# Kernel tuning notes

Hardware: AMD Instinct MI355X
Metric: run time of the kernel (lower is better)

## Reference

```python
import jax, jax.numpy as jnp
import numpy as np


def setup_inputs() -> dict:
    key = jax.random.key(0)
    k1, k2 = jax.random.split(key)
    B, N, M, D = 8, 8192, 8192, 3
    x = jax.random.normal(k1, (B, N, D), dtype=jnp.float32)
    y = jax.random.normal(k2, (B, M, D), dtype=jnp.float32)
    return {"x": x, "y": y}


def reference(x, y):
    # dist[b, i, j] = |x_bi|^2 + |y_bj|^2 - 2 * <x_bi, y_bj>
    # (same math as the torch code's rx.transpose(2,1) + ry - 2*xy, but
    #  computed with row-norm vectors instead of full NxN / MxM bmms)
    xx = jnp.sum(x * x, axis=-1)                      # [B, N]
    yy = jnp.sum(y * y, axis=-1)                      # [B, M]
    xy = jnp.einsum('bnd,bmd->bnm', x, y)             # [B, N, M]
    dist = xx[:, :, None] + yy[:, None, :] - 2.0 * xy # [B, N, M]
    dist1 = jnp.min(dist, axis=1)  # min over x points -> per-y nearest  [B, M]
    dist2 = jnp.min(dist, axis=2)  # min over y points -> per-x nearest  [B, N]
    return jnp.mean(dist1) + jnp.mean(dist2)
```

## Files before the change

kernel.cpp:

```cpp
#include <hip/hip_runtime.h>


#define B_ 8
#define N_ 8192
#define PTS (B_ * N_)
#define TPB 512

typedef short bf16x8 __attribute__((ext_vector_type(8)));
typedef float f32x16 __attribute__((ext_vector_type(16)));

__device__ __forceinline__ unsigned b16(float f) {
  unsigned u = __float_as_uint(f);
  return (u + 0x7FFFu + ((u >> 16) & 1u)) >> 16;
}
__device__ __forceinline__ float bf(unsigned h) { return __uint_as_float(h << 16); }

__device__ __forceinline__ void build_chunk(const float* __restrict__ cb,
                                            uint4* __restrict__ dst, int t) {
  const unsigned one = 0x3F80u;
#pragma unroll
  for (int q = 0; q < 2; ++q) {
    int p = t + q * TPB;
    float c0 = cb[3 * p], c1 = cb[3 * p + 1], c2 = cb[3 * p + 2];
    float nc = fmaf(c0, c0, fmaf(c1, c1, c2 * c2));
    unsigned yh0 = b16(c0), yh1 = b16(c1), yh2 = b16(c2);
    unsigned yl0 = b16(c0 - bf(yh0)), yl1 = b16(c1 - bf(yh1)), yl2 = b16(c2 - bf(yh2));
    unsigned nh = b16(nc), nl = b16(nc - bf(nh));
    int tt = p >> 5, mm = p & 31;
    dst[tt * 64 + mm]      = make_uint4(yh0 | (yh1 << 16), yh2 | (yl0 << 16),
                                        yl1 | (yl2 << 16), yh0 | (yh1 << 16));
    dst[tt * 64 + 32 + mm] = make_uint4(yh2 | (one << 16), one | (nh << 16),
                                        nl, 0u);
  }
}

__global__ __launch_bounds__(TPB, 4) void chamfer_main_k(
    const float* __restrict__ x, const float* __restrict__ y,
    float* __restrict__ gpart) {
  __shared__ uint4 ldsFrag[2][32 * 64];

  const unsigned one = 0x3F80u;
  int t = threadIdx.x, lane = t & 63, w = t >> 6;
  int b = blockIdx.x;
  int g = b >> 1;
  int hf = b & 1;
  int dir = g >> 7;
  int gg = g & 127;
  int batch = gg >> 4;
  int seg = gg & 15;
  const float* __restrict__ own  = dir ? y : x;
  const float* __restrict__ cand = dir ? x : y;

  int m = lane & 31;
  int rowBase = batch * N_ + seg * 512 + w * 64;
  bf16x8 A0, A1;
#pragma unroll
  for (int a = 0; a < 2; ++a) {
    const float* po = own + 3 * (rowBase + a * 32 + m);
    float v0 = po[0], v1 = po[1], v2 = po[2];
    float nv = fmaf(v0, v0, fmaf(v1, v1, v2 * v2));
    float a0 = -2.0f * v0, a1 = -2.0f * v1, a2 = -2.0f * v2;
    unsigned ah0 = b16(a0), ah1 = b16(a1), ah2 = b16(a2);
    unsigned al0 = b16(a0 - bf(ah0)), al1 = b16(a1 - bf(ah1)), al2 = b16(a2 - bf(ah2));
    unsigned nh = b16(nv), nl = b16(nv - bf(nh));
    uint4 h0 = make_uint4(ah0 | (ah1 << 16), ah2 | (ah0 << 16),
                          ah1 | (ah2 << 16), al0 | (al1 << 16));
    uint4 h1 = make_uint4(al2 | (nh << 16), nl | (one << 16), one, 0u);
    uint4 afr;
    afr.x = (lane < 32) ? h0.x : h1.x;
    afr.y = (lane < 32) ? h0.y : h1.y;
    afr.z = (lane < 32) ? h0.z : h1.z;
    afr.w = (lane < 32) ? h0.w : h1.w;
    if (a == 0) A0 = __builtin_bit_cast(bf16x8, afr);
    else        A1 = __builtin_bit_cast(bf16x8, afr);
  }

  f32x16 z = {0.f,0.f,0.f,0.f,0.f,0.f,0.f,0.f,0.f,0.f,0.f,0.f,0.f,0.f,0.f,0.f};
  f32x16 rm0, rm1;
#pragma unroll
  for (int r = 0; r < 16; ++r) { rm0[r] = 1e30f; rm1[r] = 1e30f; }

  const float* cbb = cand + (batch * N_ + hf * 4096) * 3;
  build_chunk(cbb, ldsFrag[0], t);
  __syncthreads();

  for (int ch = 0; ch < 4; ++ch) {
    const uint4* cur = ldsFrag[ch & 1];
    if (ch < 3)
      build_chunk(cbb + (ch + 1) * 1024 * 3, ldsFrag[(ch + 1) & 1], t);

#pragma unroll 2
    for (int i = 0; i < 16; ++i) {
      bf16x8 B0 = __builtin_bit_cast(bf16x8, cur[(2 * i) * 64 + lane]);
      bf16x8 B1 = __builtin_bit_cast(bf16x8, cur[(2 * i + 1) * 64 + lane]);
      f32x16 acc0 = __builtin_amdgcn_mfma_f32_32x32x16_bf16(A0, B0, z, 0, 0, 0);
      f32x16 acc1 = __builtin_amdgcn_mfma_f32_32x32x16_bf16(A1, B0, z, 0, 0, 0);
      f32x16 acc2 = __builtin_amdgcn_mfma_f32_32x32x16_bf16(A0, B1, z, 0, 0, 0);
      f32x16 acc3 = __builtin_amdgcn_mfma_f32_32x32x16_bf16(A1, B1, z, 0, 0, 0);
#pragma unroll
      for (int r = 0; r < 16; ++r) {
        rm0[r] = fminf(fminf(rm0[r], acc0[r]), acc2[r]);
        rm1[r] = fminf(fminf(rm1[r], acc1[r]), acc3[r]);
      }
    }
    __syncthreads();
  }

#pragma unroll
  for (int msk = 1; msk <= 16; msk <<= 1)
#pragma unroll
    for (int r = 0; r < 16; ++r) {
      rm0[r] = fminf(rm0[r], __shfl_xor(rm0[r], msk, 64));
      rm1[r] = fminf(rm1[r], __shfl_xor(rm1[r], msk, 64));
    }

  float* gp = gpart + b * 512;
  if ((lane & 31) == 0) {
    int h = lane >> 5;
#pragma unroll
    for (int r = 0; r < 16; ++r) {
      int rr = (r & 3) + 8 * (r >> 2) + 4 * h;
      gp[w * 64 + rr] = rm0[r];
      gp[w * 64 + 32 + rr] = rm1[r];
    }
  }
}

__global__ __launch_bounds__(256) void chamfer_final_k(
    const float* __restrict__ gpart, float* __restrict__ out) {
  int i = blockIdx.x * 256 + threadIdx.x;
  float s = 0.0f;
#pragma unroll
  for (int e = 0; e < 4; ++e) {
    int rowid = 4 * i + e;
    int g = rowid >> 9, r = rowid & 511;
    s += fminf(gpart[(2 * g) * 512 + r], gpart[(2 * g + 1) * 512 + r]);
  }
  for (int off = 32; off > 0; off >>= 1) s += __shfl_down(s, off, 64);
  __shared__ float red[4];
  int lane = threadIdx.x & 63, wv = threadIdx.x >> 6;
  if (lane == 0) red[wv] = s;
  __syncthreads();
  if (threadIdx.x == 0) {
    float tt = (red[0] + red[1]) + (red[2] + red[3]);
    atomicAdd(out, tt * (1.0f / (float)PTS));
  }
}

extern "C" void kernel_launch(void* const* d_in, const int* in_sizes, int n_in,
                              void* d_out, int out_size, void* d_ws, size_t ws_size,
                              hipStream_t stream) {
  const float* x = (const float*)d_in[0];
  const float* y = (const float*)d_in[1];
  float* out = (float*)d_out;
  float* gpart = (float*)d_ws;

  hipMemsetAsync(out, 0, sizeof(float), stream);
  chamfer_main_k<<<512, TPB, 0, stream>>>(x, y, gpart);
  chamfer_final_k<<<128, 256, 0, stream>>>(gpart, out);
}
```

Before: 95.30 us.

## Prepack MFMA fragments in a separate kernel and stream candidates from global memory

Adds a pack kernel that converts all points once into bf16 hi/lo MFMA fragment layouts in workspace. The main kernel then reads its A and B fragments straight from global memory (L2) instead of rebuilding candidate chunks into LDS with double buffering and barriers. Work is split four ways along the candidate axis across 2048 smaller 256-thread blocks with a swizzled block order, and the final kernel takes a four-way min using vector loads. This removes redundant per-block conversion and syncs, at the cost of an extra launch and more global/L2 traffic.

```diff
diff --git a/kernel.cpp b/kernel.cpp
--- a/kernel.cpp
+++ b/kernel.cpp
@@ -4,7 +4,9 @@
 #define B_ 8
 #define N_ 8192
 #define PTS (B_ * N_)
-#define TPB 512
+#define ROWS_TOTAL (2 * PTS)
+#define NTILES 2048
+#define TPB 256
 
 typedef short bf16x8 __attribute__((ext_vector_type(8)));
 typedef float f32x16 __attribute__((ext_vector_type(16)));
@@ -15,95 +17,76 @@
 }
 __device__ __forceinline__ float bf(unsigned h) { return __uint_as_float(h << 16); }
 
-__device__ __forceinline__ void build_chunk(const float* __restrict__ cb,
-                                            uint4* __restrict__ dst, int t) {
+__global__ __launch_bounds__(256) void pack_frags_k(
+    const float* __restrict__ x, const float* __restrict__ y,
+    uint4* __restrict__ afrag, uint4* __restrict__ bfrag) {
   const unsigned one = 0x3F80u;
-#pragma unroll
-  for (int q = 0; q < 2; ++q) {
-    int p = t + q * TPB;
-    float c0 = cb[3 * p], c1 = cb[3 * p + 1], c2 = cb[3 * p + 2];
-    float nc = fmaf(c0, c0, fmaf(c1, c1, c2 * c2));
-    unsigned yh0 = b16(c0), yh1 = b16(c1), yh2 = b16(c2);
-    unsigned yl0 = b16(c0 - bf(yh0)), yl1 = b16(c1 - bf(yh1)), yl2 = b16(c2 - bf(yh2));
-    unsigned nh = b16(nc), nl = b16(nc - bf(nh));
-    int tt = p >> 5, mm = p & 31;
-    dst[tt * 64 + mm]      = make_uint4(yh0 | (yh1 << 16), yh2 | (yl0 << 16),
-                                        yl1 | (yl2 << 16), yh0 | (yh1 << 16));
-    dst[tt * 64 + 32 + mm] = make_uint4(yh2 | (one << 16), one | (nh << 16),
-                                        nl, 0u);
-  }
-}
-
-__global__ __launch_bounds__(TPB, 4) void chamfer_main_k(
-    const float* __restrict__ x, const float* __restrict__ y,
-    float* __restrict__ gpart) {
-  __shared__ uint4 ldsFrag[2][32 * 64];
-
-  const unsigned one = 0x3F80u;
-  int t = threadIdx.x, lane = t & 63, w = t >> 6;
-  int b = blockIdx.x;
-  int g = b >> 1;
-  int hf = b & 1;
-  int dir = g >> 7;
-  int gg = g & 127;
-  int batch = gg >> 4;
-  int seg = gg & 15;
-  const float* __restrict__ own  = dir ? y : x;
-  const float* __restrict__ cand = dir ? x : y;
-
-  int m = lane & 31;
-  int rowBase = batch * N_ + seg * 512 + w * 64;
-  bf16x8 A0, A1;
-#pragma unroll
-  for (int a = 0; a < 2; ++a) {
-    const float* po = own + 3 * (rowBase + a * 32 + m);
+  int t = blockIdx.x * 256 + threadIdx.x;
+  int kind = t >> 17;
+  int dir = (t >> 16) & 1;
+  int p = t & 65535;
+  int tile = dir * NTILES + (p >> 5), m = p & 31;
+  if (kind == 0) {
+    const float* src = dir ? y : x;
+    const float* po = src + 3 * p;
     float v0 = po[0], v1 = po[1], v2 = po[2];
     float nv = fmaf(v0, v0, fmaf(v1, v1, v2 * v2));
     float a0 = -2.0f * v0, a1 = -2.0f * v1, a2 = -2.0f * v2;
     unsigned ah0 = b16(a0), ah1 = b16(a1), ah2 = b16(a2);
     unsigned al0 = b16(a0 - bf(ah0)), al1 = b16(a1 - bf(ah1)), al2 = b16(a2 - bf(ah2));
     unsigned nh = b16(nv), nl = b16(nv - bf(nh));
-    uint4 h0 = make_uint4(ah0 | (ah1 << 16), ah2 | (ah0 << 16),
-                          ah1 | (ah2 << 16), al0 | (al1 << 16));
-    uint4 h1 = make_uint4(al2 | (nh << 16), nl | (one << 16), one, 0u);
-    uint4 afr;
-    afr.x = (lane < 32) ? h0.x : h1.x;
-    afr.y = (lane < 32) ? h0.y : h1.y;
-    afr.z = (lane < 32) ? h0.z : h1.z;
-    afr.w = (lane < 32) ? h0.w : h1.w;
-    if (a == 0) A0 = __builtin_bit_cast(bf16x8, afr);
-    else        A1 = __builtin_bit_cast(bf16x8, afr);
+    afrag[tile * 64 + m]      = make_uint4(ah0 | (ah1 << 16), ah2 | (ah0 << 16),
+                                           ah1 | (ah2 << 16), al0 | (al1 << 16));
+    afrag[tile * 64 + 32 + m] = make_uint4(al2 | (nh << 16), nl | (one << 16), one, 0u);
+  } else {
+    const float* src = dir ? x : y;
+    const float* pc = src + 3 * p;
+    float c0 = pc[0], c1 = pc[1], c2 = pc[2];
+    float nc = fmaf(c0, c0, fmaf(c1, c1, c2 * c2));
+    unsigned yh0 = b16(c0), yh1 = b16(c1), yh2 = b16(c2);
+    unsigned yl0 = b16(c0 - bf(yh0)), yl1 = b16(c1 - bf(yh1)), yl2 = b16(c2 - bf(yh2));
+    unsigned nh = b16(nc), nl = b16(nc - bf(nh));
+    bfrag[tile * 64 + m]      = make_uint4(yh0 | (yh1 << 16), yh2 | (yl0 << 16),
+                                           yl1 | (yl2 << 16), yh0 | (yh1 << 16));
+    bfrag[tile * 64 + 32 + m] = make_uint4(yh2 | (one << 16), one | (nh << 16), nl, 0u);
   }
+}
 
-  f32x16 z = {0.f,0.f,0.f,0.f,0.f,0.f,0.f,0.f,0.f,0.f,0.f,0.f,0.f,0.f,0.f,0.f};
-  f32x16 rm0, rm1;
+__global__ __launch_bounds__(TPB, 3) void chamfer_main_k(
+    const uint4* __restrict__ afrag, const uint4* __restrict__ bfrag,
+    float* __restrict__ gpart) {
+  int t = threadIdx.x, lane = t & 63, w = t >> 6;
+  int b0 = blockIdx.x;
+  int eff = ((b0 & 7) << 8) | (b0 >> 3);
+  int q = eff & 3;
+  int rg = eff >> 2;
+  int dir = rg >> 8;
+  int batch = (rg >> 5) & 7;
+  int rb = rg & 31;
+
+  int tileA0 = dir * NTILES + batch * 256 + rb * 8 + w * 2;
+  bf16x8 A0 = __builtin_bit_cast(bf16x8, afrag[tileA0 * 64 + lane]);
+  bf16x8 A1 = __builtin_bit_cast(bf16x8, afrag[(tileA0 + 1) * 64 + lane]);
+
+  const uint4* bt = bfrag + (size_t)(dir * NTILES + batch * 256 + q * 64) * 64 + lane;
+
+  f32x16 z, rm0, rm1;
 #pragma unroll
-  for (int r = 0; r < 16; ++r) { rm0[r] = 1e30f; rm1[r] = 1e30f; }
-
-  const float* cbb = cand + (batch * N_ + hf * 4096) * 3;
-  build_chunk(cbb, ldsFrag[0], t);
-  __syncthreads();
-
-  for (int ch = 0; ch < 4; ++ch) {
-    const uint4* cur = ldsFrag[ch & 1];
-    if (ch < 3)
-      build_chunk(cbb + (ch + 1) * 1024 * 3, ldsFrag[(ch + 1) & 1], t);
+  for (int r = 0; r < 16; ++r) { z[r] = 0.0f; rm0[r] = 1e30f; rm1[r] = 1e30f; }
 
 #pragma unroll 2
-    for (int i = 0; i < 16; ++i) {
-      bf16x8 B0 = __builtin_bit_cast(bf16x8, cur[(2 * i) * 64 + lane]);
-      bf16x8 B1 = __builtin_bit_cast(bf16x8, cur[(2 * i + 1) * 64 + lane]);
-      f32x16 acc0 = __builtin_amdgcn_mfma_f32_32x32x16_bf16(A0, B0, z, 0, 0, 0);
-      f32x16 acc1 = __builtin_amdgcn_mfma_f32_32x32x16_bf16(A1, B0, z, 0, 0, 0);
-      f32x16 acc2 = __builtin_amdgcn_mfma_f32_32x32x16_bf16(A0, B1, z, 0, 0, 0);
-      f32x16 acc3 = __builtin_amdgcn_mfma_f32_32x32x16_bf16(A1, B1, z, 0, 0, 0);
+  for (int j = 0; j < 64; j += 2) {
+    bf16x8 B0 = __builtin_bit_cast(bf16x8, bt[(j    ) * 64]);
+    bf16x8 B1 = __builtin_bit_cast(bf16x8, bt[(j + 1) * 64]);
+    f32x16 acc0 = __builtin_amdgcn_mfma_f32_32x32x16_bf16(A0, B0, z, 0, 0, 0);
+    f32x16 acc1 = __builtin_amdgcn_mfma_f32_32x32x16_bf16(A1, B0, z, 0, 0, 0);
+    f32x16 acc2 = __builtin_amdgcn_mfma_f32_32x32x16_bf16(A0, B1, z, 0, 0, 0);
+    f32x16 acc3 = __builtin_amdgcn_mfma_f32_32x32x16_bf16(A1, B1, z, 0, 0, 0);
 #pragma unroll
-      for (int r = 0; r < 16; ++r) {
-        rm0[r] = fminf(fminf(rm0[r], acc0[r]), acc2[r]);
-        rm1[r] = fminf(fminf(rm1[r], acc1[r]), acc3[r]);
-      }
+    for (int r = 0; r < 16; ++r) {
+      rm0[r] = fminf(fminf(rm0[r], acc0[r]), acc2[r]);
+      rm1[r] = fminf(fminf(rm1[r], acc1[r]), acc3[r]);
     }
-    __syncthreads();
   }
 
 #pragma unroll
@@ -114,14 +97,15 @@
       rm1[r] = fminf(rm1[r], __shfl_xor(rm1[r], msk, 64));
     }
 
-  float* gp = gpart + b * 512;
+  int rowbase = dir * PTS + batch * N_ + rb * 256 + w * 64;
+  float* gp = gpart + q * ROWS_TOTAL + rowbase;
   if ((lane & 31) == 0) {
     int h = lane >> 5;
 #pragma unroll
     for (int r = 0; r < 16; ++r) {
       int rr = (r & 3) + 8 * (r >> 2) + 4 * h;
-      gp[w * 64 + rr] = rm0[r];
-      gp[w * 64 + 32 + rr] = rm1[r];
+      gp[rr] = rm0[r];
+      gp[32 + rr] = rm1[r];
     }
   }
 }
@@ -129,13 +113,15 @@
 __global__ __launch_bounds__(256) void chamfer_final_k(
     const float* __restrict__ gpart, float* __restrict__ out) {
   int i = blockIdx.x * 256 + threadIdx.x;
-  float s = 0.0f;
-#pragma unroll
-  for (int e = 0; e < 4; ++e) {
-    int rowid = 4 * i + e;
-    int g = rowid >> 9, r = rowid & 511;
-    s += fminf(gpart[(2 * g) * 512 + r], gpart[(2 * g + 1) * 512 + r]);
-  }
+  const float4* g4 = reinterpret_cast<const float4*>(gpart);
+  float4 a = g4[i];
+  float4 b = g4[i + (ROWS_TOTAL / 4)];
+  float4 c = g4[i + 2 * (ROWS_TOTAL / 4)];
+  float4 d = g4[i + 3 * (ROWS_TOTAL / 4)];
+  float s = fminf(fminf(a.x, b.x), fminf(c.x, d.x))
+          + fminf(fminf(a.y, b.y), fminf(c.y, d.y))
+          + fminf(fminf(a.z, b.z), fminf(c.z, d.z))
+          + fminf(fminf(a.w, b.w), fminf(c.w, d.w));
   for (int off = 32; off > 0; off >>= 1) s += __shfl_down(s, off, 64);
   __shared__ float red[4];
   int lane = threadIdx.x & 63, wv = threadIdx.x >> 6;
@@ -154,8 +140,11 @@
   const float* y = (const float*)d_in[1];
   float* out = (float*)d_out;
   float* gpart = (float*)d_ws;
+  uint4* afrag = (uint4*)((char*)d_ws + (size_t)4 * ROWS_TOTAL * sizeof(float));
+  uint4* bfrag = afrag + (size_t)2 * NTILES * 64;
 
   hipMemsetAsync(out, 0, sizeof(float), stream);
-  chamfer_main_k<<<512, TPB, 0, stream>>>(x, y, gpart);
+  pack_frags_k<<<1024, 256, 0, stream>>>(x, y, afrag, bfrag);
+  chamfer_main_k<<<2048, TPB, 0, stream>>>(afrag, bfrag, gpart);
   chamfer_final_k<<<128, 256, 0, stream>>>(gpart, out);
 }
```

Measured after the change: 103.3 us. +8.4%, slower.
